# Kernel optimization log

Measured on AMD Instinct MI355X. Metric: run time of the kernel, lower is better.

The kernel has to match this reference:

```python
import jax, jax.numpy as jnp
import numpy as np

N = 262144          # total flattened parameter count
K = 1024            # VQ codebook size (dim = 1 per original unsqueeze(-1))


def setup_inputs() -> dict:
    key = jax.random.key(0)
    k1, k2 = jax.random.split(key)
    weights = jax.random.normal(k1, (N,), dtype=jnp.float32)      # flattened state_dict
    codebook = jax.random.normal(k2, (K, 1), dtype=jnp.float32)   # frozen VQ codebook
    y = 1  # passthrough label
    return {"weights": weights, "codebook": codebook, "y": y}


def reference(weights, codebook, y):
    # TokenTransform3D.forward: flatten (already flat), unsqueeze(-1) -> [N,1],
    # VQ lookup with frozen codebook: squared-euclidean cdist + argmin.
    x = weights[:, None]                                  # [N, 1]
    # dim==1 so squared distance is just (x - c)^2; materialize [N, K] like cdist
    dist = jnp.square(x - codebook[:, 0][None, :])        # [N, K]
    indices = jnp.argmin(dist, axis=-1)                   # [N] int
    return (indices, y)
```

## Files before the change

### kernel.cpp

```cpp
#include <hip/hip_runtime.h>


#define N_W  262144
#define K_CB 1024
#define NB   256
#define BLK  1024

__device__ __forceinline__ float dsq(float x, float c) {
    float d = x - c;
    return d * d;
}

__global__ __launch_bounds__(BLK) void vq_bucket_kernel(
    const float* __restrict__ w,
    const float* __restrict__ cb,
    const int* __restrict__ y,
    int* __restrict__ out)
{
    __shared__ float bval[K_CB];
    __shared__ int   bidx[K_CB];
    __shared__ int   hist[NB];
    __shared__ int   bstart[NB + 1];
    __shared__ int   cursor[NB];
    __shared__ float wred[32];
    __shared__ float gmm[2];

    const int t    = threadIdx.x;
    const int gid  = blockIdx.x * BLK + t;
    const int lane = t & 63;
    const int wid  = t >> 6;

    float x = w[gid];
    float c = cb[t];

    float m = c, M = c;
    #pragma unroll
    for (int off = 32; off >= 1; off >>= 1) {
        m = fminf(m, __shfl_xor(m, off));
        M = fmaxf(M, __shfl_xor(M, off));
    }
    if (lane == 0) { wred[wid] = m; wred[16 + wid] = M; }
    if (t < NB) hist[t] = 0;
    __syncthreads();
    if (t == 0) {
        float mm = wred[0], MM = wred[16];
        for (int i = 1; i < 16; ++i) {
            mm = fminf(mm, wred[i]);
            MM = fmaxf(MM, wred[16 + i]);
        }
        gmm[0] = mm; gmm[1] = MM;
    }
    __syncthreads();
    const float gmin  = gmm[0], gmax = gmm[1];
    const float range = gmax - gmin;
    const bool  degen = !(range > 0.0f);
    const float inv   = degen ? 0.0f : ((float)NB / range);
    const float width = degen ? 0.0f : (range / (float)NB);

    int cbb = (int)((c - gmin) * inv);
    cbb = min(max(cbb, 0), NB - 1);
    atomicAdd(&hist[cbb], 1);
    __syncthreads();

    if (wid == 0) {
        int h0 = hist[4 * lane + 0], h1 = hist[4 * lane + 1];
        int h2 = hist[4 * lane + 2], h3 = hist[4 * lane + 3];
        int s1 = h0 + h1, s2 = s1 + h2, tot = s2 + h3;
        int inc = tot;
        #pragma unroll
        for (int off = 1; off < 64; off <<= 1) {
            int v = __shfl_up(inc, off);
            if (lane >= off) inc += v;
        }
        int exc = inc - tot;
        bstart[4 * lane + 0] = exc;       cursor[4 * lane + 0] = exc;
        bstart[4 * lane + 1] = exc + h0;  cursor[4 * lane + 1] = exc + h0;
        bstart[4 * lane + 2] = exc + s1;  cursor[4 * lane + 2] = exc + s1;
        bstart[4 * lane + 3] = exc + s2;  cursor[4 * lane + 3] = exc + s2;
        if (lane == 63) bstart[NB] = inc;
    }
    __syncthreads();

    int pos = atomicAdd(&cursor[cbb], 1);
    bval[pos] = c;
    bidx[pos] = t;
    __syncthreads();

    int b = (int)((x - gmin) * inv);
    b = min(max(b, 0), NB - 1);

    float best = __builtin_inff();
    int   bi   = 0x7fffffff;

    {
        int e = bstart[b + 1];
        for (int i = bstart[b]; i < e; ++i) {
            float d = dsq(x, bval[i]);
            int idx = bidx[i];
            if (d < best)                { best = d; bi = idx; }
            else if (d == best && idx < bi) { bi = idx; }
        }
    }

    int  dl = b - 1, dr = b + 1;
    bool goL = !degen && (dl >= 0);
    bool goR = !degen && (dr < NB);
    while (goL || goR) {
        if (goL) {
            float edge = gmin + (float)(dl + 2) * width;
            float gap  = x - edge;
            if (gap > 0.0f && gap * gap > best) {
                goL = false;
            } else {
                int e = bstart[dl + 1];
                for (int i = bstart[dl]; i < e; ++i) {
                    float d = dsq(x, bval[i]);
                    int idx = bidx[i];
                    if (d < best)                { best = d; bi = idx; }
                    else if (d == best && idx < bi) { bi = idx; }
                }
                if (--dl < 0) goL = false;
            }
        }
        if (goR) {
            float edge = gmin + (float)(dr - 1) * width;
            float gap  = edge - x;
            if (gap > 0.0f && gap * gap > best) {
                goR = false;
            } else {
                int e = bstart[dr + 1];
                for (int i = bstart[dr]; i < e; ++i) {
                    float d = dsq(x, bval[i]);
                    int idx = bidx[i];
                    if (d < best)                { best = d; bi = idx; }
                    else if (d == best && idx < bi) { bi = idx; }
                }
                if (++dr >= NB) goR = false;
            }
        }
    }
    if (bi == 0x7fffffff) bi = 0;
    out[gid] = bi;

    if (gid == 0) out[N_W] = y[0];
}

extern "C" void kernel_launch(void* const* d_in, const int* in_sizes, int n_in,
                              void* d_out, int out_size, void* d_ws, size_t ws_size,
                              hipStream_t stream) {
    const float* w  = (const float*)d_in[0];
    const float* cb = (const float*)d_in[1];
    const int*   y  = (const int*)d_in[2];
    int* out = (int*)d_out;

    (void)d_ws; (void)ws_size;

    vq_bucket_kernel<<<N_W / BLK, BLK, 0, stream>>>(w, cb, y, out);
}
```

Baseline: 16.35 us.

## Use fixed bucket range and smaller blocks with vectorized codebook bucketing

Drops the per-block min/max reduction over the codebook and uses a hardcoded bucket range of [-4.2, 4.2] instead. Block size shrinks from 1024 to 256 threads, and each thread loads four codebook entries as a float4 and inserts them into the shared-memory buckets. This removes a reduction and two barriers and allows smaller blocks. In exchange, each of the four times as many blocks rebuilds the full codebook bucket structure. Clamping values outside the fixed range keeps results exact, but search cost depends on the inputs fitting that range.

```diff
diff --git a/kernel.cpp b/kernel.cpp
--- a/kernel.cpp
+++ b/kernel.cpp
@@ -4,14 +4,18 @@
 #define N_W  262144
 #define K_CB 1024
 #define NB   256
-#define BLK  1024
+#define BLK  256
+#define GRID (N_W / BLK)
+
+#define GLO   (-4.2f)
+#define GRANGE (8.4f)
 
 __device__ __forceinline__ float dsq(float x, float c) {
     float d = x - c;
     return d * d;
 }
 
-__global__ __launch_bounds__(BLK) void vq_bucket_kernel(
+__global__ __launch_bounds__(BLK) void vq_grid_kernel(
     const float* __restrict__ w,
     const float* __restrict__ cb,
     const int* __restrict__ y,
@@ -22,72 +26,58 @@
     __shared__ int   hist[NB];
     __shared__ int   bstart[NB + 1];
     __shared__ int   cursor[NB];
-    __shared__ float wred[32];
-    __shared__ float gmm[2];
 
-    const int t    = threadIdx.x;
-    const int gid  = blockIdx.x * BLK + t;
-    const int lane = t & 63;
-    const int wid  = t >> 6;
+    const int t   = threadIdx.x;
+    const int gid = blockIdx.x * BLK + t;
+
+    const float inv = (float)NB / GRANGE;
+    const float wdt = GRANGE / (float)NB;
 
     float x = w[gid];
-    float c = cb[t];
+    const float4 c4 = reinterpret_cast<const float4*>(cb)[t];
 
-    float m = c, M = c;
-    #pragma unroll
-    for (int off = 32; off >= 1; off >>= 1) {
-        m = fminf(m, __shfl_xor(m, off));
-        M = fmaxf(M, __shfl_xor(M, off));
-    }
-    if (lane == 0) { wred[wid] = m; wred[16 + wid] = M; }
-    if (t < NB) hist[t] = 0;
-    __syncthreads();
-    if (t == 0) {
-        float mm = wred[0], MM = wred[16];
-        for (int i = 1; i < 16; ++i) {
-            mm = fminf(mm, wred[i]);
-            MM = fmaxf(MM, wred[16 + i]);
-        }
-        gmm[0] = mm; gmm[1] = MM;
-    }
-    __syncthreads();
-    const float gmin  = gmm[0], gmax = gmm[1];
-    const float range = gmax - gmin;
-    const bool  degen = !(range > 0.0f);
-    const float inv   = degen ? 0.0f : ((float)NB / range);
-    const float width = degen ? 0.0f : (range / (float)NB);
-
-    int cbb = (int)((c - gmin) * inv);
-    cbb = min(max(cbb, 0), NB - 1);
-    atomicAdd(&hist[cbb], 1);
+    hist[t] = 0;
     __syncthreads();
 
-    if (wid == 0) {
-        int h0 = hist[4 * lane + 0], h1 = hist[4 * lane + 1];
-        int h2 = hist[4 * lane + 2], h3 = hist[4 * lane + 3];
+    int b0 = min(max((int)((c4.x - GLO) * inv), 0), NB - 1);
+    int b1 = min(max((int)((c4.y - GLO) * inv), 0), NB - 1);
+    int b2 = min(max((int)((c4.z - GLO) * inv), 0), NB - 1);
+    int b3 = min(max((int)((c4.w - GLO) * inv), 0), NB - 1);
+    atomicAdd(&hist[b0], 1);
+    atomicAdd(&hist[b1], 1);
+    atomicAdd(&hist[b2], 1);
+    atomicAdd(&hist[b3], 1);
+    __syncthreads();
+
+    if (t < 64) {
+        int h0 = hist[4 * t + 0], h1 = hist[4 * t + 1];
+        int h2 = hist[4 * t + 2], h3 = hist[4 * t + 3];
         int s1 = h0 + h1, s2 = s1 + h2, tot = s2 + h3;
         int inc = tot;
         #pragma unroll
         for (int off = 1; off < 64; off <<= 1) {
             int v = __shfl_up(inc, off);
-            if (lane >= off) inc += v;
+            if (t >= off) inc += v;
         }
         int exc = inc - tot;
-        bstart[4 * lane + 0] = exc;       cursor[4 * lane + 0] = exc;
-        bstart[4 * lane + 1] = exc + h0;  cursor[4 * lane + 1] = exc + h0;
-        bstart[4 * lane + 2] = exc + s1;  cursor[4 * lane + 2] = exc + s1;
-        bstart[4 * lane + 3] = exc + s2;  cursor[4 * lane + 3] = exc + s2;
-        if (lane == 63) bstart[NB] = inc;
+        bstart[4 * t + 0] = exc;      cursor[4 * t + 0] = exc;
+        bstart[4 * t + 1] = exc + h0; cursor[4 * t + 1] = exc + h0;
+        bstart[4 * t + 2] = exc + s1; cursor[4 * t + 2] = exc + s1;
+        bstart[4 * t + 3] = exc + s2; cursor[4 * t + 3] = exc + s2;
+        if (t == 63) bstart[NB] = inc;
     }
     __syncthreads();
 
-    int pos = atomicAdd(&cursor[cbb], 1);
-    bval[pos] = c;
-    bidx[pos] = t;
+    {
+        int p;
+        p = atomicAdd(&cursor[b0], 1); bval[p] = c4.x; bidx[p] = 4 * t + 0;
+        p = atomicAdd(&cursor[b1], 1); bval[p] = c4.y; bidx[p] = 4 * t + 1;
+        p = atomicAdd(&cursor[b2], 1); bval[p] = c4.z; bidx[p] = 4 * t + 2;
+        p = atomicAdd(&cursor[b3], 1); bval[p] = c4.w; bidx[p] = 4 * t + 3;
+    }
     __syncthreads();
 
-    int b = (int)((x - gmin) * inv);
-    b = min(max(b, 0), NB - 1);
+    int b = min(max((int)((x - GLO) * inv), 0), NB - 1);
 
     float best = __builtin_inff();
     int   bi   = 0x7fffffff;
@@ -97,17 +87,17 @@
         for (int i = bstart[b]; i < e; ++i) {
             float d = dsq(x, bval[i]);
             int idx = bidx[i];
-            if (d < best)                { best = d; bi = idx; }
+            if (d < best)                   { best = d; bi = idx; }
             else if (d == best && idx < bi) { bi = idx; }
         }
     }
 
     int  dl = b - 1, dr = b + 1;
-    bool goL = !degen && (dl >= 0);
-    bool goR = !degen && (dr < NB);
+    bool goL = (dl >= 0);
+    bool goR = (dr < NB);
     while (goL || goR) {
         if (goL) {
-            float edge = gmin + (float)(dl + 2) * width;
+            float edge = GLO + (float)(dl + 2) * wdt;
             float gap  = x - edge;
             if (gap > 0.0f && gap * gap > best) {
                 goL = false;
@@ -116,14 +106,14 @@
                 for (int i = bstart[dl]; i < e; ++i) {
                     float d = dsq(x, bval[i]);
                     int idx = bidx[i];
-                    if (d < best)                { best = d; bi = idx; }
+                    if (d < best)                   { best = d; bi = idx; }
                     else if (d == best && idx < bi) { bi = idx; }
                 }
                 if (--dl < 0) goL = false;
             }
         }
         if (goR) {
-            float edge = gmin + (float)(dr - 1) * width;
+            float edge = GLO + (float)(dr - 1) * wdt;
             float gap  = edge - x;
             if (gap > 0.0f && gap * gap > best) {
                 goR = false;
@@ -132,7 +122,7 @@
                 for (int i = bstart[dr]; i < e; ++i) {
                     float d = dsq(x, bval[i]);
                     int idx = bidx[i];
-                    if (d < best)                { best = d; bi = idx; }
+                    if (d < best)                   { best = d; bi = idx; }
                     else if (d == best && idx < bi) { bi = idx; }
                 }
                 if (++dr >= NB) goR = false;
@@ -155,5 +145,5 @@
 
     (void)d_ws; (void)ws_size;
 
-    vq_bucket_kernel<<<N_W / BLK, BLK, 0, stream>>>(w, cb, y, out);
+    vq_grid_kernel<<<GRID, BLK, 0, stream>>>(w, cb, y, out);
 }
```

After: 20.67 us. 1.26x slower.
